# Performance work log

Measured on AMD Instinct MI355X. Metric: run time of the kernel, lower is better.

Reference implementation:

```python
import jax, jax.numpy as jnp
import numpy as np

N = 100000   # nodes
E = 1600000  # edges
D = 128      # in = hidden = out channels


def _gcn_norm(edge_index):
    # PyG gcn_norm with improved=True: add self-loops with weight 2.0,
    # symmetric normalization deg^{-1/2} A deg^{-1/2}.
    src, dst = edge_index[0], edge_index[1]
    loop = jnp.arange(N, dtype=src.dtype)
    src = jnp.concatenate([src, loop])
    dst = jnp.concatenate([dst, loop])
    w = jnp.concatenate([jnp.ones((E,), jnp.float32), jnp.full((N,), 2.0, jnp.float32)])
    deg = jax.ops.segment_sum(w, dst, num_segments=N)
    dinv = jnp.where(deg > 0, jax.lax.rsqrt(deg), 0.0)
    norm = dinv[src] * w * dinv[dst]  # [E+N]
    return src, dst, norm


def _gcn_conv(x, src, dst, norm, W, b):
    h = x @ W                                   # [N, D] dense transform
    msg = h[src] * norm[:, None]                # gather + scale  [E+N, D]
    agg = jax.ops.segment_sum(msg, dst, num_segments=N)  # scatter-add
    return agg + b


def setup_inputs() -> dict:
    key = jax.random.key(0)
    ks = jax.random.split(key, 8)
    scale = 1.0 / np.sqrt(D)
    inp = {
        "x": jax.random.normal(ks[0], (N, D), jnp.float32),
        "edge_index": jax.random.randint(ks[1], (2, E), 0, N, dtype=jnp.int32),
        "W0": jax.random.normal(ks[2], (D, D), jnp.float32) * scale,
        "b0": jnp.zeros((D,), jnp.float32),
        "W1": jax.random.normal(ks[3], (D, D), jnp.float32) * scale,
        "b1": jnp.zeros((D,), jnp.float32),
        "W2": jax.random.normal(ks[4], (D, D), jnp.float32) * scale,
        "b2": jnp.zeros((D,), jnp.float32),
    }
    return inp


def reference(x, edge_index, W0, b0, W1, b1, W2, b2):
    src, dst, norm = _gcn_norm(edge_index)
    global_identity = x
    out = x
    for W, b in ((W0, b0), (W1, b1), (W2, b2)):
        inter_identity = out
        out = _gcn_conv(out, src, dst, norm, W, b)  # inter_act = identity
        out = out + inter_identity                   # inter residual
    out = out + global_identity                      # global residual
    return out                                        # out_act = identity
```

## Files before the change

kernel.cpp:

```cpp
#include <hip/hip_runtime.h>

#define NN 100000
#define NE 1600000
#define DD 128

typedef short short8 __attribute__((ext_vector_type(8)));
typedef float f32x4 __attribute__((ext_vector_type(4)));


__device__ __forceinline__ unsigned short f2bf(float f) {
    union { float f; unsigned u; } v; v.f = f;
    unsigned r = v.u + 0x7FFF + ((v.u >> 16) & 1);
    return (unsigned short)(r >> 16);
}
__device__ __forceinline__ float bf2f(unsigned short b) {
    union { unsigned u; float f; } v; v.u = (unsigned)b << 16;
    return v.f;
}


__global__ __launch_bounds__(256) void k_count(const int* __restrict__ dstA,
                                               int* __restrict__ cnt, int E) {
    int i = blockIdx.x * 256 + threadIdx.x;
    if (i < E) atomicAdd(&cnt[dstA[i]], 1);
}

__global__ __launch_bounds__(256) void k_scan1(int* __restrict__ rowp,
                                               float* __restrict__ dinv,
                                               int* __restrict__ bsum, int N) {
    __shared__ int sm[256];
    int tid = threadIdx.x;
    int i = blockIdx.x * 256 + tid;
    int v = (i < N) ? rowp[1 + i] : 0;
    if (i < N) dinv[i] = rsqrtf(2.0f + (float)v);
    sm[tid] = v;
    #pragma unroll
    for (int off = 1; off < 256; off <<= 1) {
        __syncthreads();
        int t = (tid >= off) ? sm[tid - off] : 0;
        __syncthreads();
        sm[tid] += t;
    }
    if (i < N) rowp[1 + i] = sm[tid];
    if (tid == 255) bsum[blockIdx.x] = sm[255];
}

__global__ __launch_bounds__(512) void k_scan2(int* __restrict__ bsum, int nb) {
    __shared__ int sm[512];
    int tid = threadIdx.x;
    sm[tid] = (tid < nb) ? bsum[tid] : 0;
    #pragma unroll
    for (int off = 1; off < 512; off <<= 1) {
        __syncthreads();
        int t = (tid >= off) ? sm[tid - off] : 0;
        __syncthreads();
        sm[tid] += t;
    }
    if (tid < nb) bsum[tid] = sm[tid];
}

__global__ __launch_bounds__(256) void k_scan3(int* __restrict__ rowp,
                                               const int* __restrict__ bsum,
                                               int* __restrict__ bcur, int N) {
    int tid = threadIdx.x;
    int i = blockIdx.x * 256 + tid;
    if (i >= N) return;
    int add = (blockIdx.x > 0) ? bsum[blockIdx.x - 1] : 0;
    int fin = rowp[1 + i] + add;
    rowp[1 + i] = fin;
    if (i == 0) bcur[0] = 0;
    if (((i + 1) & 127) == 0 && (i + 1) < N) bcur[(i + 1) >> 7] = fin;
}

__global__ __launch_bounds__(256) void k_part(const int* __restrict__ srcA,
                                              const int* __restrict__ dstA,
                                              int* __restrict__ bcur,
                                              uint2* __restrict__ tmp, int E, int NBk) {
    __shared__ int cur[1024];
    int tid = threadIdx.x;
    int chunk = (E + gridDim.x - 1) / gridDim.x;
    int e0 = blockIdx.x * chunk;
    int e1 = e0 + chunk; e1 = e1 < E ? e1 : E;
    if (e0 >= e1) return;

    for (int b = tid; b < NBk; b += 256) cur[b] = 0;
    __syncthreads();
    for (int i = e0 + tid; i < e1; i += 256)
        atomicAdd(&cur[dstA[i] >> 7], 1);
    __syncthreads();
    for (int b = tid; b < NBk; b += 256) {
        int c = cur[b];
        cur[b] = (c > 0) ? atomicAdd(&bcur[b], c) : 0;
    }
    __syncthreads();
    for (int i = e0 + tid; i < e1; i += 256) {
        int s = srcA[i], d = dstA[i];
        int slot = atomicAdd(&cur[d >> 7], 1);
        uint2 p; p.x = (unsigned)s; p.y = (unsigned)d;
        tmp[slot] = p;
    }
}

__global__ __launch_bounds__(256) void k_place(const uint2* __restrict__ tmp,
                                               const int* __restrict__ rowp,
                                               int* __restrict__ col, int N) {
    __shared__ int lcur[128];
    int b = blockIdx.x;
    int n0 = b << 7;
    int tid = threadIdx.x;
    int nEnd = n0 + 128; nEnd = nEnd < N ? nEnd : N;
    int base = rowp[n0];
    int cnt = rowp[nEnd] - base;
    if (tid < 128) {
        int node = n0 + tid;
        lcur[tid] = (node < N) ? (rowp[node] - base) : 0;
    }
    __syncthreads();
    for (int i = tid; i < cnt; i += 256) {
        uint2 p = tmp[base + i];
        int j = (int)p.y - n0;
        int slot = atomicAdd(&lcur[j], 1);
        col[base + slot] = (int)p.x;
    }
}

__global__ __launch_bounds__(256) void k_prep(const float* __restrict__ W0,
                                              const float* __restrict__ W1,
                                              const float* __restrict__ W2,
                                              unsigned short* __restrict__ wt) {
    int layer = blockIdx.x >> 6;
    int idx = (blockIdx.x & 63) * 256 + threadIdx.x;
    const float* W = (layer == 0) ? W0 : (layer == 1) ? W1 : W2;
    char* dstB = (char*)(wt + (size_t)layer * 16384);
    int k = idx >> 7, n = idx & 127;
    int ba = (n * 256 + 2 * k) ^ ((n & 7) << 4);
    *(unsigned short*)(dstB + ba) = f2bf(W[idx]);
}


template <int BF16A>
__global__ __launch_bounds__(512) void k_gemm(const void* __restrict__ Fv,
                                              const unsigned short* __restrict__ wt,
                                              unsigned short* __restrict__ Hb, int N) {
    __shared__ char Wl[34816];
    int tid = threadIdx.x;

    {
        const uint4* src = reinterpret_cast<const uint4*>(wt);
        uint4* dst = reinterpret_cast<uint4*>(Wl);
        #pragma unroll
        for (int i = 0; i < 4; ++i) dst[tid + 512 * i] = src[tid + 512 * i];
    }
    __syncthreads();

    int wv = tid >> 6;
    int l  = tid & 63;
    int nn = l & 15;
    int g  = l >> 4;
    int r0w = blockIdx.x * 128 + wv * 16;

    int row = r0w + nn;
    row = row < N ? row : N - 1;

    f32x4 acc[8];
    #pragma unroll
    for (int nt = 0; nt < 8; ++nt) acc[nt] = (f32x4){0.f, 0.f, 0.f, 0.f};

    #pragma unroll
    for (int ks = 0; ks < 4; ++ks) {
        short8 a;
        if (BF16A) {
            const char* Fb = (const char*)Fv + (size_t)row * 256;
            a = *(const short8*)(Fb + ks * 64 + g * 16);
        } else {
            const float4* Fr = reinterpret_cast<const float4*>((const float*)Fv + (size_t)row * DD);
            float4 f0 = Fr[ks * 8 + g * 2];
            float4 f1 = Fr[ks * 8 + g * 2 + 1];
            a[0] = (short)f2bf(f0.x); a[1] = (short)f2bf(f0.y);
            a[2] = (short)f2bf(f0.z); a[3] = (short)f2bf(f0.w);
            a[4] = (short)f2bf(f1.x); a[5] = (short)f2bf(f1.y);
            a[6] = (short)f2bf(f1.z); a[7] = (short)f2bf(f1.w);
        }
        #pragma unroll
        for (int nt = 0; nt < 8; ++nt) {
            int ba = ((nt * 16 + nn) * 256 + ks * 64 + g * 16) ^ ((nn & 7) << 4);
            short8 b = *(const short8*)(Wl + ba);
            acc[nt] = __builtin_amdgcn_mfma_f32_16x16x32_bf16(a, b, acc[nt], 0, 0, 0);
        }
    }

    __syncthreads();

    #pragma unroll
    for (int nt = 0; nt < 8; ++nt) {
        #pragma unroll
        for (int j = 0; j < 4; ++j) {
            int r = wv * 16 + 4 * g + j;
            *(unsigned short*)(Wl + r * 272 + (nt * 16 + nn) * 2) = f2bf(acc[nt][j]);
        }
    }
    __syncthreads();

    #pragma unroll
    for (int it = 0; it < 4; ++it) {
        int idx = it * 512 + tid;
        int r = idx >> 4, ch = idx & 15;
        int gr = blockIdx.x * 128 + r;
        if (gr < N) {
            uint4 v = *(const uint4*)(Wl + r * 272 + ch * 16);
            *reinterpret_cast<uint4*>(&Hb[(size_t)gr * DD + ch * 8]) = v;
        }
    }
}


template <int RBF16, int OBF16, int ADDX>
__global__ __launch_bounds__(256) void k_agg(const unsigned short* __restrict__ Hb,
                                             const int* __restrict__ rowp,
                                             const int* __restrict__ col,
                                             const float* __restrict__ dinv,
                                             const float* __restrict__ bias,
                                             const void* __restrict__ resv,
                                             const float* __restrict__ X,
                                             void* __restrict__ outv, int N) {
    int lane = threadIdx.x & 63;
    int n = (blockIdx.x << 2) + (threadIdx.x >> 6);
    if (n >= N) return;
    int c = lane << 1;
    size_t base = (size_t)n * DD + c;

    float di = dinv[n];
    unsigned hv = *reinterpret_cast<const unsigned*>(&Hb[base]);
    float s2 = 2.f * di * di;
    float sx = s2 * bf2f((unsigned short)(hv & 0xffff));
    float sy = s2 * bf2f((unsigned short)(hv >> 16));
    float ax = 0.f, ay = 0.f;

    int e = rowp[n], e1 = rowp[n + 1];
    for (; e + 8 <= e1; e += 8) {
        int s[8];
        float w[8];
        unsigned gg[8];
        #pragma unroll
        for (int j = 0; j < 8; ++j) s[j] = col[e + j];
        #pragma unroll
        for (int j = 0; j < 8; ++j) w[j] = dinv[s[j]];
        #pragma unroll
        for (int j = 0; j < 8; ++j)
            gg[j] = *reinterpret_cast<const unsigned*>(&Hb[(size_t)s[j] * DD + c]);
        #pragma unroll
        for (int j = 0; j < 8; ++j) {
            ax += w[j] * bf2f((unsigned short)(gg[j] & 0xffff));
            ay += w[j] * bf2f((unsigned short)(gg[j] >> 16));
        }
    }
    for (; e + 2 <= e1; e += 2) {
        int s0 = col[e], s1 = col[e + 1];
        float w0 = dinv[s0], w1 = dinv[s1];
        unsigned g0 = *reinterpret_cast<const unsigned*>(&Hb[(size_t)s0 * DD + c]);
        unsigned g1 = *reinterpret_cast<const unsigned*>(&Hb[(size_t)s1 * DD + c]);
        ax += w0 * bf2f((unsigned short)(g0 & 0xffff)) + w1 * bf2f((unsigned short)(g1 & 0xffff));
        ay += w0 * bf2f((unsigned short)(g0 >> 16))    + w1 * bf2f((unsigned short)(g1 >> 16));
    }
    if (e < e1) {
        int s0 = col[e];
        float w0 = dinv[s0];
        unsigned g0 = *reinterpret_cast<const unsigned*>(&Hb[(size_t)s0 * DD + c]);
        ax += w0 * bf2f((unsigned short)(g0 & 0xffff));
        ay += w0 * bf2f((unsigned short)(g0 >> 16));
    }

    float rx, ry;
    if (RBF16) {
        const unsigned short* R = (const unsigned short*)resv;
        unsigned rv = *reinterpret_cast<const unsigned*>(&R[base]);
        rx = bf2f((unsigned short)(rv & 0xffff));
        ry = bf2f((unsigned short)(rv >> 16));
    } else {
        const float* R = (const float*)resv;
        float2 fv = *reinterpret_cast<const float2*>(&R[base]);
        rx = fv.x; ry = fv.y;
    }
    float2 bv = *reinterpret_cast<const float2*>(&bias[c]);
    float ox = di * ax + sx + bv.x + rx;
    float oy = di * ay + sy + bv.y + ry;
    if (ADDX) {
        float2 xv = *reinterpret_cast<const float2*>(&X[base]);
        ox += xv.x;
        oy += xv.y;
    }
    if (OBF16) {
        unsigned short* O = (unsigned short*)outv;
        unsigned pv = (unsigned)f2bf(ox) | ((unsigned)f2bf(oy) << 16);
        *reinterpret_cast<unsigned*>(&O[base]) = pv;
    } else {
        float* O = (float*)outv;
        float2 o; o.x = ox; o.y = oy;
        *reinterpret_cast<float2*>(&O[base]) = o;
    }
}


extern "C" void kernel_launch(void* const* d_in, const int* in_sizes, int n_in,
                              void* d_out, int out_size, void* d_ws, size_t ws_size,
                              hipStream_t stream) {
    const float* x  = (const float*)d_in[0];
    const int*   ei = (const int*)d_in[1];
    const float* W0 = (const float*)d_in[2];
    const float* b0 = (const float*)d_in[3];
    const float* W1 = (const float*)d_in[4];
    const float* b1 = (const float*)d_in[5];
    const float* W2 = (const float*)d_in[6];
    const float* b2 = (const float*)d_in[7];
    float* out = (float*)d_out;

    const int N = NN, E = NE;
    const int* srcA = ei;
    const int* dstA = ei + E;

    char* ws = (char*)d_ws;
    size_t off = 0;
    auto alloc = [&](size_t bytes) -> char* {
        char* p = ws + off;
        off += (bytes + 255) & ~size_t(255);
        return p;
    };
    int*   rowp   = (int*)  alloc((size_t)(N + 1) * sizeof(int));
    int*   bcur   = (int*)  alloc(1024 * sizeof(int));
    int*   bsum   = (int*)  alloc(512 * sizeof(int));
    float* dinv   = (float*)alloc((size_t)N * sizeof(float));
    int*   col    = (int*)  alloc((size_t)E * sizeof(int));
    unsigned short* wt = (unsigned short*)alloc(3 * 32768);
    unsigned short* ob = (unsigned short*)alloc((size_t)N * DD * sizeof(unsigned short));
    size_t tmpBytes = (size_t)E * sizeof(uint2);
    size_t hBytes   = (size_t)N * DD * sizeof(unsigned short);
    char*  uni = alloc(tmpBytes > hBytes ? tmpBytes : hBytes);
    uint2* tmp = (uint2*)uni;
    unsigned short* h = (unsigned short*)uni;
    (void)ws_size; (void)in_sizes; (void)n_in; (void)out_size;

    hipMemsetAsync(rowp, 0, (size_t)(N + 1) * sizeof(int), stream);

    int gE = (E + 255) / 256;
    int gN = (N + 255) / 256;
    int NB = (N + 127) / 128;
    k_count<<<gE, 256, 0, stream>>>(dstA, rowp + 1, E);
    k_prep <<<192, 256, 0, stream>>>(W0, W1, W2, wt);
    k_scan1<<<gN, 256, 0, stream>>>(rowp, dinv, bsum, N);
    k_scan2<<<1, 512, 0, stream>>>(bsum, gN);
    k_scan3<<<gN, 256, 0, stream>>>(rowp, bsum, bcur, N);
    k_part <<<512, 256, 0, stream>>>(srcA, dstA, bcur, tmp, E, NB);
    k_place<<<NB, 256, 0, stream>>>(tmp, rowp, col, N);

    int gG = (N + 127) / 128;
    int gA = (N + 3) / 4;

    k_gemm<0><<<gG, 512, 0, stream>>>(x, wt, h, N);
    k_agg<0, 1, 0><<<gA, 256, 0, stream>>>(h, rowp, col, dinv, b0, x, nullptr, ob, N);
    k_gemm<1><<<gG, 512, 0, stream>>>(ob, wt + 16384, h, N);
    k_agg<1, 1, 0><<<gA, 256, 0, stream>>>(h, rowp, col, dinv, b1, ob, nullptr, ob, N);
    k_gemm<1><<<gG, 512, 0, stream>>>(ob, wt + 32768, h, N);
    k_agg<1, 0, 1><<<gA, 256, 0, stream>>>(h, rowp, col, dinv, b2, ob, x, out, N);
}
```

Measured before the change: 383.9 us.

## Replace per-node degree count and three-pass scan with bucket histogram CSR build

Removes the global per-node atomic degree count and the three-kernel prefix scan over all nodes. A shared-memory histogram of 128-node buckets and a single-block bucket scan drive the partition step. Per-node degrees, row pointers and dinv are then computed inside k_place from a local shared histogram and scan. This cuts global atomics and kernel launches in the CSR preprocessing, at the cost of an extra pass over tmp inside k_place.

```diff
diff --git a/kernel.cpp b/kernel.cpp
--- a/kernel.cpp
+++ b/kernel.cpp
@@ -19,57 +19,45 @@
 }
 
 
-__global__ __launch_bounds__(256) void k_count(const int* __restrict__ dstA,
-                                               int* __restrict__ cnt, int E) {
-    int i = blockIdx.x * 256 + threadIdx.x;
-    if (i < E) atomicAdd(&cnt[dstA[i]], 1);
-}
-
-__global__ __launch_bounds__(256) void k_scan1(int* __restrict__ rowp,
-                                               float* __restrict__ dinv,
-                                               int* __restrict__ bsum, int N) {
-    __shared__ int sm[256];
-    int tid = threadIdx.x;
-    int i = blockIdx.x * 256 + tid;
-    int v = (i < N) ? rowp[1 + i] : 0;
-    if (i < N) dinv[i] = rsqrtf(2.0f + (float)v);
-    sm[tid] = v;
-    #pragma unroll
-    for (int off = 1; off < 256; off <<= 1) {
+__global__ __launch_bounds__(256) void k_bhist(const int* __restrict__ dstA,
+                                               int* __restrict__ bcnt, int E, int NBk) {
+    __shared__ int h[1024];
+    int tid = threadIdx.x;
+    int chunk = (E + gridDim.x - 1) / gridDim.x;
+    int e0 = blockIdx.x * chunk;
+    int e1 = e0 + chunk; e1 = e1 < E ? e1 : E;
+    for (int b = tid; b < NBk; b += 256) h[b] = 0;
+    __syncthreads();
+    for (int i = e0 + tid; i < e1; i += 256)
+        atomicAdd(&h[dstA[i] >> 7], 1);
+    __syncthreads();
+    for (int b = tid; b < NBk; b += 256) {
+        int c = h[b];
+        if (c > 0) atomicAdd(&bcnt[b], c);
+    }
+}
+
+__global__ __launch_bounds__(1024) void k_bscan(const int* __restrict__ bcnt,
+                                                int* __restrict__ bbase,
+                                                int* __restrict__ bcur, int NBk, int E) {
+    __shared__ int sm[1024];
+    int tid = threadIdx.x;
+    int own = (tid < NBk) ? bcnt[tid] : 0;
+    sm[tid] = own;
+    #pragma unroll
+    for (int off = 1; off < 1024; off <<= 1) {
         __syncthreads();
         int t = (tid >= off) ? sm[tid - off] : 0;
         __syncthreads();
         sm[tid] += t;
     }
-    if (i < N) rowp[1 + i] = sm[tid];
-    if (tid == 255) bsum[blockIdx.x] = sm[255];
-}
-
-__global__ __launch_bounds__(512) void k_scan2(int* __restrict__ bsum, int nb) {
-    __shared__ int sm[512];
-    int tid = threadIdx.x;
-    sm[tid] = (tid < nb) ? bsum[tid] : 0;
-    #pragma unroll
-    for (int off = 1; off < 512; off <<= 1) {
-        __syncthreads();
-        int t = (tid >= off) ? sm[tid - off] : 0;
-        __syncthreads();
-        sm[tid] += t;
-    }
-    if (tid < nb) bsum[tid] = sm[tid];
-}
-
-__global__ __launch_bounds__(256) void k_scan3(int* __restrict__ rowp,
-                                               const int* __restrict__ bsum,
-                                               int* __restrict__ bcur, int N) {
-    int tid = threadIdx.x;
-    int i = blockIdx.x * 256 + tid;
-    if (i >= N) return;
-    int add = (blockIdx.x > 0) ? bsum[blockIdx.x - 1] : 0;
-    int fin = rowp[1 + i] + add;
-    rowp[1 + i] = fin;
-    if (i == 0) bcur[0] = 0;
-    if (((i + 1) & 127) == 0 && (i + 1) < N) bcur[(i + 1) >> 7] = fin;
+    __syncthreads();
+    if (tid < NBk) {
+        int ex = sm[tid] - own;
+        bbase[tid] = ex;
+        bcur[tid] = ex;
+    }
+    if (tid == 0) bbase[NBk] = E;
 }
 
 __global__ __launch_bounds__(256) void k_part(const int* __restrict__ srcA,
@@ -102,19 +90,45 @@
 }
 
 __global__ __launch_bounds__(256) void k_place(const uint2* __restrict__ tmp,
-                                               const int* __restrict__ rowp,
-                                               int* __restrict__ col, int N) {
+                                               const int* __restrict__ bbase,
+                                               int* __restrict__ rowp,
+                                               float* __restrict__ dinv,
+                                               int* __restrict__ col,
+                                               int N, int NBk, int E) {
+    __shared__ int hist[128];
     __shared__ int lcur[128];
     int b = blockIdx.x;
     int n0 = b << 7;
     int tid = threadIdx.x;
-    int nEnd = n0 + 128; nEnd = nEnd < N ? nEnd : N;
-    int base = rowp[n0];
-    int cnt = rowp[nEnd] - base;
+    int base = bbase[b];
+    int cnt = bbase[b + 1] - base;
+
+    if (tid < 128) hist[tid] = 0;
+    __syncthreads();
+    for (int i = tid; i < cnt; i += 256)
+        atomicAdd(&hist[(int)tmp[base + i].y - n0], 1);
+    __syncthreads();
+    if (tid < 128) lcur[tid] = hist[tid];
+    #pragma unroll
+    for (int off = 1; off < 128; off <<= 1) {
+        __syncthreads();
+        int t = (tid >= off && tid < 128) ? lcur[tid - off] : 0;
+        __syncthreads();
+        if (tid < 128) lcur[tid] += t;
+    }
+    __syncthreads();
+    int pref = 0;
     if (tid < 128) {
+        pref = lcur[tid] - hist[tid];
         int node = n0 + tid;
-        lcur[tid] = (node < N) ? (rowp[node] - base) : 0;
-    }
+        if (node < N) {
+            rowp[node] = base + pref;
+            dinv[node] = rsqrtf(2.0f + (float)hist[tid]);
+        }
+    }
+    __syncthreads();
+    if (tid < 128) lcur[tid] = pref;
+    if (b == NBk - 1 && tid == 0) rowp[N] = E;
     __syncthreads();
     for (int i = tid; i < cnt; i += 256) {
         uint2 p = tmp[base + i];
@@ -136,7 +150,6 @@
     int ba = (n * 256 + 2 * k) ^ ((n & 7) << 4);
     *(unsigned short*)(dstB + ba) = f2bf(W[idx]);
 }
-
 
 template <int BF16A>
 __global__ __launch_bounds__(512) void k_gemm(const void* __restrict__ Fv,
@@ -326,8 +339,9 @@
         return p;
     };
     int*   rowp   = (int*)  alloc((size_t)(N + 1) * sizeof(int));
+    int*   bcnt   = (int*)  alloc(1024 * sizeof(int));
+    int*   bbase  = (int*)  alloc(1025 * sizeof(int));
     int*   bcur   = (int*)  alloc(1024 * sizeof(int));
-    int*   bsum   = (int*)  alloc(512 * sizeof(int));
     float* dinv   = (float*)alloc((size_t)N * sizeof(float));
     int*   col    = (int*)  alloc((size_t)E * sizeof(int));
     unsigned short* wt = (unsigned short*)alloc(3 * 32768);
@@ -339,18 +353,14 @@
     unsigned short* h = (unsigned short*)uni;
     (void)ws_size; (void)in_sizes; (void)n_in; (void)out_size;
 
-    hipMemsetAsync(rowp, 0, (size_t)(N + 1) * sizeof(int), stream);
-
-    int gE = (E + 255) / 256;
-    int gN = (N + 255) / 256;
-    int NB = (N + 127) / 128;
-    k_count<<<gE, 256, 0, stream>>>(dstA, rowp + 1, E);
+    const int NB = (N + 127) / 128;
+    hipMemsetAsync(bcnt, 0, 1024 * sizeof(int), stream);
+
     k_prep <<<192, 256, 0, stream>>>(W0, W1, W2, wt);
-    k_scan1<<<gN, 256, 0, stream>>>(rowp, dinv, bsum, N);
-    k_scan2<<<1, 512, 0, stream>>>(bsum, gN);
-    k_scan3<<<gN, 256, 0, stream>>>(rowp, bsum, bcur, N);
+    k_bhist<<<512, 256, 0, stream>>>(dstA, bcnt, E, NB);
+    k_bscan<<<1, 1024, 0, stream>>>(bcnt, bbase, bcur, NB, E);
     k_part <<<512, 256, 0, stream>>>(srcA, dstA, bcur, tmp, E, NB);
-    k_place<<<NB, 256, 0, stream>>>(tmp, rowp, col, N);
+    k_place<<<NB, 256, 0, stream>>>(tmp, bbase, rowp, dinv, col, N, NB, E);
 
     int gG = (N + 127) / 128;
     int gA = (N + 3) / 4;
```

After: 331.3 us. 13.7% less time.
